# Kernel tuning notes

Hardware: AMD Instinct MI355X
Metric: run time of the kernel (lower is better)

## Reference

```python
import jax, jax.numpy as jnp
import numpy as np

NUM_HEADS, NUM_KEYS, NUM_VALUES, NUM_OUTPUTS = 8, 64, 64, 512
B, H, W, C = 16, 64, 64, 512


def setup_inputs() -> dict:
    key = jax.random.key(0)
    ks = jax.random.split(key, 5)
    def xavier(k, shape):
        fan_in, fan_out = shape
        lim = np.sqrt(6.0 / (fan_in + fan_out))
        return jax.random.uniform(k, shape, jnp.float32, -lim, lim)
    return {
        "x": jax.random.normal(ks[0], (B, H, W, C), jnp.float32),
        "Wq": xavier(ks[1], (C, NUM_HEADS * NUM_KEYS)),
        "bq": jnp.zeros((NUM_HEADS * NUM_KEYS,), jnp.float32),
        "Wk": xavier(ks[2], (C, NUM_HEADS * NUM_KEYS)),
        "bk": jnp.zeros((NUM_HEADS * NUM_KEYS,), jnp.float32),
        "Wv": xavier(ks[3], (C, NUM_HEADS * NUM_VALUES)),
        "bv": jnp.zeros((NUM_HEADS * NUM_VALUES,), jnp.float32),
        "Wo": xavier(ks[4], (NUM_VALUES, NUM_OUTPUTS)),
        "bo": jnp.zeros((NUM_OUTPUTS,), jnp.float32),
    }


def reference(x, Wq, bq, Wk, bk, Wv, bv, Wo, bo):
    b, h, w, c = x.shape
    n, dk, dv = NUM_HEADS, NUM_KEYS, NUM_VALUES
    # single pooled query per image
    q = (jnp.mean(x, axis=(1, 2)) @ Wq + bq).reshape(b, n, dk)      # [B,N,dk]
    K = (x @ Wk + bk).reshape(b, h, w, n, dk)                        # [B,H,W,N,dk]
    V = (x @ Wv + bv).reshape(b, h, w, n, dv)                        # [B,H,W,N,dv]
    scale = 1.0 / jnp.sqrt(jnp.float32(dk))
    # scores of the single query against every pixel
    s = jnp.einsum('bnk,bhwnk->bnhw', q, K) * scale                  # [B,N,H,W]
    attn_h = jax.nn.softmax(s, axis=-1)   # per row, softmax over width
    attn_v = jax.nn.softmax(s, axis=-2)   # per column, softmax over height
    A_h = jnp.einsum('bnhw,bhwnv->bnhv', attn_h, V)                  # [B,N,H,dv]
    A_v = jnp.einsum('bnhw,bhwnv->bnwv', attn_v, V)                  # [B,N,W,dv]
    # outer-product combine over spatial dims, summed over heads
    A = jnp.einsum('bnhv,bnwv->bhwv', A_h, A_v)                      # [B,H,W,dv]
    return A @ Wo + bo                                               # [B,H,W,num_outputs]
```

## Files before the change

kernel.cpp:

```cpp
#include <hip/hip_runtime.h>
#include <hip/hip_bf16.h>

#define NHEADS 8
#define DK 64
#define DV 64
#define CIN 512
#define PIX_PER_IMG 4096
#define NPIX 65536

typedef short bf16x8 __attribute__((ext_vector_type(8)));
typedef float f32x4 __attribute__((ext_vector_type(4)));

__device__ __forceinline__ float b2f(unsigned int u) {
  union { unsigned int i; float f; } v; v.i = u << 16; return v.f;
}
__device__ __forceinline__ unsigned short f2b(float f) {
  union { float f; unsigned int i; } v; v.f = f;
  unsigned int x = v.i;
  return (unsigned short)((x + 0x7fffu + ((x >> 16) & 1u)) >> 16);
}
__device__ __forceinline__ void gload_lds16(const void* g, void* l) {
  __builtin_amdgcn_global_load_lds(
      (const __attribute__((address_space(1))) void*)g,
      (__attribute__((address_space(3))) void*)l, 16, 0, 0);
}

__global__ void k_pool_convert(const float* __restrict__ x,
                               unsigned short* __restrict__ xb,
                               float* __restrict__ partial) {
  int blk = blockIdx.x;
  int b = blk >> 6, chunk = blk & 63;
  int t = threadIdx.x;
  int c4 = t & 127;
  int half = t >> 7;
  size_t rowbase = (size_t)b * PIX_PER_IMG + chunk * 64;
  const float4* x4 = (const float4*)x;
  float4 acc = make_float4(0.f, 0.f, 0.f, 0.f);
#pragma unroll 4
  for (int i = 0; i < 32; ++i) {
    int p = 2 * i + half;
    float4 v = x4[(rowbase + p) * 128 + c4];
    acc.x += v.x; acc.y += v.y; acc.z += v.z; acc.w += v.w;
    uint2 o;
    o.x = (unsigned)f2b(v.x) | ((unsigned)f2b(v.y) << 16);
    o.y = (unsigned)f2b(v.z) | ((unsigned)f2b(v.w) << 16);
    *(uint2*)(xb + (rowbase + p) * CIN + c4 * 4) = o;
  }
  *(float4*)(partial + ((size_t)(blk * 2 + half)) * CIN + c4 * 4) = acc;
}

__global__ void k_qp2(const float* __restrict__ partial,
                      const float* __restrict__ Wq, const float* __restrict__ bq,
                      const float* __restrict__ Wk, const float* __restrict__ bk,
                      float* __restrict__ P, float* __restrict__ s0) {
  __shared__ float xs[CIN];
  __shared__ float red[256];
  __shared__ float qsh[64];
  int b = blockIdx.x, n = blockIdx.y, t = threadIdx.x;
  for (int c = t; c < CIN; c += 256) {
    float s = 0.f;
    for (int ch = 0; ch < 128; ++ch) s += partial[((size_t)(b * 128 + ch)) * CIN + c];
    xs[c] = s * (1.0f / 4096.0f);
  }
  __syncthreads();
  int jj = t & 63, part = t >> 6;
  {
    float acc = 0.f;
    const float* wp = Wq + (size_t)(part * 128) * CIN + n * 64 + jj;
    for (int ci = 0; ci < 128; ++ci)
      acc += xs[part * 128 + ci] * wp[(size_t)ci * CIN];
    red[t] = acc;
  }
  __syncthreads();
  if (t < 64)
    qsh[t] = red[t] + red[t + 64] + red[t + 128] + red[t + 192] + bq[n * 64 + t];
  __syncthreads();
  if (t == 0) {
    float s = 0.f;
    for (int k = 0; k < 64; ++k) s += qsh[k] * bk[n * 64 + k];
    s0[b * NHEADS + n] = s;
  }
  for (int c = t; c < CIN; c += 256) {
    float acc = 0.f;
    const float* wr = Wk + (size_t)c * CIN + n * 64;
    for (int k = 0; k < 64; ++k) acc += qsh[k] * wr[k];
    P[((size_t)(b * NHEADS + n)) * CIN + c] = acc;
  }
}

__global__ void k_prep_w(const float* __restrict__ Wv, const float* __restrict__ Wo,
                         unsigned short* __restrict__ WvT, unsigned short* __restrict__ WoT) {
  int idx = blockIdx.x * 256 + threadIdx.x;
  if (idx < 262144) {
    int n = idx >> 9, c = idx & 511;
    WvT[idx] = f2b(Wv[(size_t)c * 512 + n]);
  } else {
    int j = idx - 262144;
    int o = j >> 6, kk = j & 63;
    WoT[j] = f2b(Wo[(size_t)kk * 512 + o]);
  }
}

__global__ void k_scores(const unsigned short* __restrict__ xb,
                         const float* __restrict__ P, const float* __restrict__ s0,
                         float* __restrict__ s) {
  __shared__ float Pl[NHEADS * 516];
  __shared__ float s0l[NHEADS];
  int blk = blockIdx.x;
  int b = blk >> 7, tile = blk & 127;
  int t = threadIdx.x;
  for (int idx = t; idx < NHEADS * CIN; idx += 256) {
    int n = idx >> 9, c = idx & 511;
    Pl[n * 516 + c] = P[((size_t)(b * NHEADS + n)) * CIN + c];
  }
  if (t < NHEADS) s0l[t] = s0[b * NHEADS + t];
  __syncthreads();
  int pl = t >> 3, n = t & 7;
  int pix = tile * 32 + pl;
  const uint4* xr = (const uint4*)(xb + ((size_t)b * PIX_PER_IMG + pix) * CIN);
  const float* Pr = Pl + n * 516;
  float acc = s0l[n];
  for (int cc = 0; cc < 64; ++cc) {
    uint4 u = xr[cc];
    int c = cc * 8;
    acc += b2f(u.x & 0xffff) * Pr[c + 0];
    acc += b2f(u.x >> 16) * Pr[c + 1];
    acc += b2f(u.y & 0xffff) * Pr[c + 2];
    acc += b2f(u.y >> 16) * Pr[c + 3];
    acc += b2f(u.z & 0xffff) * Pr[c + 4];
    acc += b2f(u.z >> 16) * Pr[c + 5];
    acc += b2f(u.w & 0xffff) * Pr[c + 6];
    acc += b2f(u.w >> 16) * Pr[c + 7];
  }
  s[((size_t)(b * NHEADS + n)) * PIX_PER_IMG + pix] = acc * 0.125f;
}

__global__ void k_softmax(const float* __restrict__ s,
                          float* __restrict__ ah, float* __restrict__ avT) {
  __shared__ float st[4096];
  int bn = blockIdx.x, t = threadIdx.x;
  const float* sp = s + (size_t)bn * 4096;
  for (int i = t; i < 4096; i += 256) st[i] = sp[i];
  __syncthreads();
  if (t < 64) {
    int h = t;
    float m = -1e30f;
    for (int w = 0; w < 64; ++w) m = fmaxf(m, st[h * 64 + w]);
    float sum = 0.f;
    for (int w = 0; w < 64; ++w) sum += __expf(st[h * 64 + w] - m);
    float inv = 1.f / sum;
    for (int w = 0; w < 64; ++w)
      ah[(size_t)bn * 4096 + h * 64 + w] = __expf(st[h * 64 + w] - m) * inv;
  } else if (t < 128) {
    int w = t - 64;
    float m = -1e30f;
    for (int h = 0; h < 64; ++h) m = fmaxf(m, st[h * 64 + w]);
    float sum = 0.f;
    for (int h = 0; h < 64; ++h) sum += __expf(st[h * 64 + w] - m);
    float inv = 1.f / sum;
    for (int h = 0; h < 64; ++h)
      avT[(size_t)bn * 4096 + w * 64 + h] = __expf(st[h * 64 + w] - m) * inv;
  }
}

__global__ void k_xh(const unsigned short* __restrict__ xb,
                     const float* __restrict__ ahg,
                     unsigned short* __restrict__ XHV) {
  __shared__ unsigned short xs[64 * 256];
  __shared__ float ahl[NHEADS * 64];
  int bh = blockIdx.x, ch = blockIdx.y, t = threadIdx.x;
  int b = bh >> 6, h = bh & 63;
  const unsigned short* src = xb + ((size_t)(b * PIX_PER_IMG + h * 64)) * CIN + ch * 256;
#pragma unroll
  for (int i = 0; i < 8; ++i) {
    int idx = i * 256 + t;
    int w = idx >> 5, off = idx & 31;
    ((uint4*)xs)[idx] = ((const uint4*)(src + (size_t)w * CIN))[off];
  }
#pragma unroll
  for (int i = 0; i < 2; ++i) {
    int idx = i * 256 + t;
    ahl[idx] = ahg[((size_t)(b * NHEADS + (idx >> 6))) * PIX_PER_IMG + h * 64 + (idx & 63)];
  }
  __syncthreads();
  int n = t >> 5, oct = t & 31;
  float acc[8] = {0.f, 0.f, 0.f, 0.f, 0.f, 0.f, 0.f, 0.f};
  const float* ar = ahl + n * 64;
  for (int w = 0; w < 64; ++w) {
    float aw = ar[w];
    uint4 u = *(const uint4*)(xs + (size_t)w * 256 + oct * 8);
    acc[0] += aw * b2f(u.x & 0xffff);
    acc[1] += aw * b2f(u.x >> 16);
    acc[2] += aw * b2f(u.y & 0xffff);
    acc[3] += aw * b2f(u.y >> 16);
    acc[4] += aw * b2f(u.z & 0xffff);
    acc[5] += aw * b2f(u.z >> 16);
    acc[6] += aw * b2f(u.w & 0xffff);
    acc[7] += aw * b2f(u.w >> 16);
  }
  uint4 o;
  o.x = (unsigned)f2b(acc[0]) | ((unsigned)f2b(acc[1]) << 16);
  o.y = (unsigned)f2b(acc[2]) | ((unsigned)f2b(acc[3]) << 16);
  o.z = (unsigned)f2b(acc[4]) | ((unsigned)f2b(acc[5]) << 16);
  o.w = (unsigned)f2b(acc[6]) | ((unsigned)f2b(acc[7]) << 16);
  size_t dst = ((size_t)(n * 2048 + b * 64 + h)) * CIN + ch * 256 + oct * 8;
  *(uint4*)(XHV + dst) = o;
}

__global__ void k_xv(const unsigned short* __restrict__ xb,
                     const float* __restrict__ avTg,
                     unsigned short* __restrict__ XHV) {
  __shared__ unsigned short xs[64 * 256];
  __shared__ float avl[NHEADS * 64];
  int bw = blockIdx.x, ch = blockIdx.y, t = threadIdx.x;
  int b = bw >> 6, w = bw & 63;
#pragma unroll
  for (int i = 0; i < 8; ++i) {
    int idx = i * 256 + t;
    int h = idx >> 5, off = idx & 31;
    ((uint4*)xs)[idx] =
        ((const uint4*)(xb + ((size_t)(b * PIX_PER_IMG + h * 64 + w)) * CIN + ch * 256))[off];
  }
#pragma unroll
  for (int i = 0; i < 2; ++i) {
    int idx = i * 256 + t;
    avl[idx] = avTg[((size_t)(b * NHEADS + (idx >> 6))) * PIX_PER_IMG + w * 64 + (idx & 63)];
  }
  __syncthreads();
  int n = t >> 5, oct = t & 31;
  float acc[8] = {0.f, 0.f, 0.f, 0.f, 0.f, 0.f, 0.f, 0.f};
  const float* ar = avl + n * 64;
  for (int h = 0; h < 64; ++h) {
    float aw = ar[h];
    uint4 u = *(const uint4*)(xs + (size_t)h * 256 + oct * 8);
    acc[0] += aw * b2f(u.x & 0xffff);
    acc[1] += aw * b2f(u.x >> 16);
    acc[2] += aw * b2f(u.y & 0xffff);
    acc[3] += aw * b2f(u.y >> 16);
    acc[4] += aw * b2f(u.z & 0xffff);
    acc[5] += aw * b2f(u.z >> 16);
    acc[6] += aw * b2f(u.w & 0xffff);
    acc[7] += aw * b2f(u.w >> 16);
  }
  uint4 o;
  o.x = (unsigned)f2b(acc[0]) | ((unsigned)f2b(acc[1]) << 16);
  o.y = (unsigned)f2b(acc[2]) | ((unsigned)f2b(acc[3]) << 16);
  o.z = (unsigned)f2b(acc[4]) | ((unsigned)f2b(acc[5]) << 16);
  o.w = (unsigned)f2b(acc[6]) | ((unsigned)f2b(acc[7]) << 16);
  size_t dst = ((size_t)(n * 2048 + 1024 + b * 64 + w)) * CIN + ch * 256 + oct * 8;
  *(uint4*)(XHV + dst) = o;
}

__global__ void k_gemm2(const unsigned short* __restrict__ XHV,
                        const unsigned short* __restrict__ WvT,
                        const float* __restrict__ bv,
                        float* __restrict__ Ah, float* __restrict__ Av) {
  __shared__ __align__(16) unsigned short As[128 * 64];
  __shared__ __align__(16) unsigned short Bs[64 * 64];
  const int t = threadIdx.x;
  const int wave = t >> 6, lane = t & 63;
  const int mtile = blockIdx.x, head = blockIdx.y;
  const int m0 = mtile * 128;
  const unsigned short* A = XHV + (size_t)head * 2048 * CIN;
  const unsigned short* BT = WvT + (size_t)head * 64 * CIN;

  f32x4 acc[2][4];
  for (int i = 0; i < 2; ++i)
    for (int j = 0; j < 4; ++j) acc[i][j] = (f32x4){0.f, 0.f, 0.f, 0.f};

  const int lrow = wave * 8 + (lane >> 3);
  const int lcolb = (lane & 7) * 16;

  for (int kt = 0; kt < 8; ++kt) {
    __syncthreads();
#pragma unroll
    for (int j = 0; j < 4; ++j) {
      gload_lds16((const char*)A + ((size_t)(m0 + j * 32 + lrow) * CIN + kt * 64) * 2 + lcolb,
                  (char*)As + (j * 32 + wave * 8) * 128);
    }
#pragma unroll
    for (int j = 0; j < 2; ++j) {
      gload_lds16((const char*)BT + ((size_t)(j * 32 + lrow) * CIN + kt * 64) * 2 + lcolb,
                  (char*)Bs + (j * 32 + wave * 8) * 128);
    }
    __syncthreads();
#pragma unroll
    for (int s = 0; s < 2; ++s) {
      bf16x8 af[2], bg[4];
#pragma unroll
      for (int i = 0; i < 2; ++i) {
        int mrow = wave * 32 + i * 16 + (lane & 15);
        af[i] = *(const bf16x8*)((const char*)As + mrow * 128 + s * 64 + ((lane >> 4) * 16));
      }
#pragma unroll
      for (int j = 0; j < 4; ++j) {
        int nrow = j * 16 + (lane & 15);
        bg[j] = *(const bf16x8*)((const char*)Bs + nrow * 128 + s * 64 + ((lane >> 4) * 16));
      }
#pragma unroll
      for (int i = 0; i < 2; ++i)
#pragma unroll
        for (int j = 0; j < 4; ++j)
          acc[i][j] = __builtin_amdgcn_mfma_f32_16x16x32_bf16(af[i], bg[j], acc[i][j], 0, 0, 0);
    }
  }
#pragma unroll
  for (int i = 0; i < 2; ++i)
#pragma unroll
    for (int j = 0; j < 4; ++j) {
      int v = j * 16 + (lane & 15);
      float bb = bv[head * 64 + v];
#pragma unroll
      for (int r = 0; r < 4; ++r) {
        int m = m0 + wave * 32 + i * 16 + ((lane >> 4) * 4) + r;
        float val = acc[i][j][r] + bb;
        if (m < 1024) {
          int b = m >> 6, h = m & 63;
          Ah[((size_t)(b * NHEADS + head)) * 4096 + h * 64 + v] = val;
        } else {
          int m2 = m - 1024;
          int b = m2 >> 6, w = m2 & 63;
          Av[((size_t)(b * NHEADS + head)) * 4096 + w * 64 + v] = val;
        }
      }
    }
}

__global__ void k_outgemm(const float* __restrict__ Ah, const float* __restrict__ Av,
                          const unsigned short* __restrict__ WoT,
                          const float* __restrict__ bo, float* __restrict__ out) {
  __shared__ __align__(16) unsigned short As[128 * 64];
  __shared__ __align__(16) unsigned short Bs[128 * 64];
  const int t = threadIdx.x;
  const int wave = t >> 6, lane = t & 63;
  const int wr = wave >> 1, wc = wave & 1;
  const int m0 = blockIdx.y * 128, n0 = blockIdx.x * 128;
  const int b = m0 >> 12, h0 = (m0 >> 6) & 63;

  const int srow = wave * 32 + (lane >> 3), scolb = (lane & 7) * 16;
#pragma unroll
  for (int j = 0; j < 4; ++j)
    gload_lds16((const char*)WoT + ((size_t)(n0 + srow + j * 8) * 64) * 2 + scolb,
                (char*)Bs + wave * 4096 + j * 1024);

  {
    const int v = t & 63, rg = t >> 6;
    float ahv0[8], ahv1[8];
#pragma unroll
    for (int n = 0; n < 8; ++n) {
      ahv0[n] = Ah[((size_t)((b * 8 + n) * 64 + h0)) * 64 + v];
      ahv1[n] = Ah[((size_t)((b * 8 + n) * 64 + h0 + 1)) * 64 + v];
    }
#pragma unroll 2
    for (int i = 0; i < 16; ++i) {
      int w = rg * 16 + i;
      float a0 = 0.f, a1 = 0.f;
#pragma unroll
      for (int n = 0; n < 8; ++n) {
        float av = Av[((size_t)((b * 8 + n) * 64 + w)) * 64 + v];
        a0 += ahv0[n] * av;
        a1 += ahv1[n] * av;
      }
      As[w * 64 + v] = f2b(a0);
      As[(64 + w) * 64 + v] = f2b(a1);
    }
  }
  __syncthreads();

  f32x4 acc[4][4];
  for (int i = 0; i < 4; ++i)
    for (int j = 0; j < 4; ++j) acc[i][j] = (f32x4){0.f, 0.f, 0.f, 0.f};
#pragma unroll
  for (int s = 0; s < 2; ++s) {
    bf16x8 af[4], bg[4];
#pragma unroll
    for (int i = 0; i < 4; ++i) {
      int mrow = wr * 64 + i * 16 + (lane & 15);
      af[i] = *(const bf16x8*)((const char*)As + mrow * 128 + s * 64 + ((lane >> 4) * 16));
    }
#pragma unroll
    for (int j = 0; j < 4; ++j) {
      int nrow = wc * 64 + j * 16 + (lane & 15);
      bg[j] = *(const bf16x8*)((const char*)Bs + nrow * 128 + s * 64 + ((lane >> 4) * 16));
    }
#pragma unroll
    for (int i = 0; i < 4; ++i)
#pragma unroll
      for (int j = 0; j < 4; ++j)
        acc[i][j] = __builtin_amdgcn_mfma_f32_16x16x32_bf16(af[i], bg[j], acc[i][j], 0, 0, 0);
  }
#pragma unroll
  for (int i = 0; i < 4; ++i)
#pragma unroll
    for (int j = 0; j < 4; ++j) {
      int mbase = m0 + wr * 64 + i * 16 + ((lane >> 4) * 4);
      int n = n0 + wc * 64 + j * 16 + (lane & 15);
      float bb = bo[n];
#pragma unroll
      for (int r = 0; r < 4; ++r)
        out[(size_t)(mbase + r) * 512 + n] = acc[i][j][r] + bb;
    }
}

extern "C" void kernel_launch(void* const* d_in, const int* in_sizes, int n_in,
                              void* d_out, int out_size, void* d_ws, size_t ws_size,
                              hipStream_t stream) {
  (void)in_sizes; (void)n_in; (void)out_size; (void)ws_size;
  const float* x = (const float*)d_in[0];
  const float* Wq = (const float*)d_in[1];
  const float* bq = (const float*)d_in[2];
  const float* Wk = (const float*)d_in[3];
  const float* bk = (const float*)d_in[4];
  const float* Wv = (const float*)d_in[5];
  const float* bv = (const float*)d_in[6];
  const float* Wo = (const float*)d_in[7];
  const float* bo = (const float*)d_in[8];
  float* out = (float*)d_out;

  char* ws = (char*)d_ws;
  unsigned short* xb = (unsigned short*)(ws + 0);
  float* s = (float*)(ws + 67108864);
  float* partial = (float*)(ws + 69206016);
  float* P = (float*)(ws + 73400320);
  float* s0 = (float*)(ws + 73662464);
  float* attn_h = (float*)(ws + 73662976);
  float* avT = (float*)(ws + 75760128);
  unsigned short* XHV = (unsigned short*)(ws + 77857280);
  float* Ah = (float*)(ws + 94634496);
  float* Av = (float*)(ws + 96731648);
  unsigned short* WvT = (unsigned short*)(ws + 98828800);
  unsigned short* WoT = (unsigned short*)(ws + 99353088);

  k_pool_convert<<<1024, 256, 0, stream>>>(x, xb, partial);
  k_qp2<<<dim3(16, 8), 256, 0, stream>>>(partial, Wq, bq, Wk, bk, P, s0);
  k_prep_w<<<1152, 256, 0, stream>>>(Wv, Wo, WvT, WoT);
  k_scores<<<2048, 256, 0, stream>>>(xb, P, s0, s);
  k_softmax<<<128, 256, 0, stream>>>(s, attn_h, avT);
  k_xh<<<dim3(1024, 2), 256, 0, stream>>>(xb, attn_h, XHV);
  k_xv<<<dim3(1024, 2), 256, 0, stream>>>(xb, avT, XHV);
  k_gemm2<<<dim3(16, 8), 256, 0, stream>>>(XHV, WvT, bv, Ah, Av);
  k_outgemm<<<dim3(4, 512), 256, 0, stream>>>(Ah, Av, WoT, bo, out);
}
```

Measured before the change: 370.9 us.

## Use MFMA split-bf16 for scores, merge launches, parallelize softmax

Computes attention scores with bf16 MFMA using a hi/lo split of the projected query to keep precision, replacing the scalar dot-product loop. It merges weight prep into the pooling kernel and the row and column weighted-sum kernels into one launch, which cuts launch count. Softmax now uses 256 threads with register buffers and shuffle reductions instead of 128 serial threads. The bk-dependent constant is dropped because softmax is invariant to a per-row shift. The hi/lo split doubles MFMA work, and the scores still read x only in bf16.

```diff
diff --git a/kernel.cpp b/kernel.cpp
--- a/kernel.cpp
+++ b/kernel.cpp
@@ -25,19 +25,33 @@
       (__attribute__((address_space(3))) void*)l, 16, 0, 0);
 }
 
-__global__ void k_pool_convert(const float* __restrict__ x,
-                               unsigned short* __restrict__ xb,
-                               float* __restrict__ partial) {
+__global__ __launch_bounds__(256) void k_pool_prep(
+    const float* __restrict__ x, unsigned short* __restrict__ xb,
+    float* __restrict__ partial,
+    const float* __restrict__ Wv, const float* __restrict__ Wo,
+    unsigned short* __restrict__ WvT, unsigned short* __restrict__ WoT) {
   int blk = blockIdx.x;
-  int b = blk >> 6, chunk = blk & 63;
   int t = threadIdx.x;
+  if (blk >= 2048) {
+    int idx = (blk - 2048) * 256 + t;
+    if (idx < 262144) {
+      int n = idx >> 9, c = idx & 511;
+      WvT[idx] = f2b(Wv[(size_t)c * 512 + n]);
+    } else {
+      int j = idx - 262144;
+      int o = j >> 6, kk = j & 63;
+      WoT[j] = f2b(Wo[(size_t)kk * 512 + o]);
+    }
+    return;
+  }
+  int b = blk >> 7, chunk = blk & 127;
   int c4 = t & 127;
   int half = t >> 7;
-  size_t rowbase = (size_t)b * PIX_PER_IMG + chunk * 64;
+  size_t rowbase = (size_t)b * PIX_PER_IMG + chunk * 32;
   const float4* x4 = (const float4*)x;
   float4 acc = make_float4(0.f, 0.f, 0.f, 0.f);
-#pragma unroll 4
-  for (int i = 0; i < 32; ++i) {
+#pragma unroll
+  for (int i = 0; i < 16; ++i) {
     int p = 2 * i + half;
     float4 v = x4[(rowbase + p) * 128 + c4];
     acc.x += v.x; acc.y += v.y; acc.z += v.z; acc.w += v.w;
@@ -49,17 +63,17 @@
   *(float4*)(partial + ((size_t)(blk * 2 + half)) * CIN + c4 * 4) = acc;
 }
 
-__global__ void k_qp2(const float* __restrict__ partial,
-                      const float* __restrict__ Wq, const float* __restrict__ bq,
-                      const float* __restrict__ Wk, const float* __restrict__ bk,
-                      float* __restrict__ P, float* __restrict__ s0) {
+__global__ __launch_bounds__(256) void k_qp2(
+    const float* __restrict__ partial,
+    const float* __restrict__ Wq, const float* __restrict__ bq,
+    const float* __restrict__ Wk, float* __restrict__ P) {
   __shared__ float xs[CIN];
   __shared__ float red[256];
   __shared__ float qsh[64];
   int b = blockIdx.x, n = blockIdx.y, t = threadIdx.x;
   for (int c = t; c < CIN; c += 256) {
     float s = 0.f;
-    for (int ch = 0; ch < 128; ++ch) s += partial[((size_t)(b * 128 + ch)) * CIN + c];
+    for (int ch = 0; ch < 256; ++ch) s += partial[((size_t)(b * 256 + ch)) * CIN + c];
     xs[c] = s * (1.0f / 4096.0f);
   }
   __syncthreads();
@@ -75,11 +89,6 @@
   if (t < 64)
     qsh[t] = red[t] + red[t + 64] + red[t + 128] + red[t + 192] + bq[n * 64 + t];
   __syncthreads();
-  if (t == 0) {
-    float s = 0.f;
-    for (int k = 0; k < 64; ++k) s += qsh[k] * bk[n * 64 + k];
-    s0[b * NHEADS + n] = s;
-  }
   for (int c = t; c < CIN; c += 256) {
     float acc = 0.f;
     const float* wr = Wk + (size_t)c * CIN + n * 64;
@@ -88,107 +97,113 @@
   }
 }
 
-__global__ void k_prep_w(const float* __restrict__ Wv, const float* __restrict__ Wo,
-                         unsigned short* __restrict__ WvT, unsigned short* __restrict__ WoT) {
-  int idx = blockIdx.x * 256 + threadIdx.x;
-  if (idx < 262144) {
-    int n = idx >> 9, c = idx & 511;
-    WvT[idx] = f2b(Wv[(size_t)c * 512 + n]);
-  } else {
-    int j = idx - 262144;
-    int o = j >> 6, kk = j & 63;
-    WoT[j] = f2b(Wo[(size_t)kk * 512 + o]);
-  }
-}
-
-__global__ void k_scores(const unsigned short* __restrict__ xb,
-                         const float* __restrict__ P, const float* __restrict__ s0,
-                         float* __restrict__ s) {
-  __shared__ float Pl[NHEADS * 516];
-  __shared__ float s0l[NHEADS];
+__global__ __launch_bounds__(256) void k_scores(
+    const unsigned short* __restrict__ xb, const float* __restrict__ P,
+    float* __restrict__ s) {
+  __shared__ __align__(16) unsigned short Pl[24 * 520];
   int blk = blockIdx.x;
-  int b = blk >> 7, tile = blk & 127;
+  int b = blk >> 6, tile = blk & 63;
   int t = threadIdx.x;
-  for (int idx = t; idx < NHEADS * CIN; idx += 256) {
-    int n = idx >> 9, c = idx & 511;
-    Pl[n * 516 + c] = P[((size_t)(b * NHEADS + n)) * CIN + c];
-  }
-  if (t < NHEADS) s0l[t] = s0[b * NHEADS + t];
-  __syncthreads();
-  int pl = t >> 3, n = t & 7;
-  int pix = tile * 32 + pl;
-  const uint4* xr = (const uint4*)(xb + ((size_t)b * PIX_PER_IMG + pix) * CIN);
-  const float* Pr = Pl + n * 516;
-  float acc = s0l[n];
-  for (int cc = 0; cc < 64; ++cc) {
-    uint4 u = xr[cc];
-    int c = cc * 8;
-    acc += b2f(u.x & 0xffff) * Pr[c + 0];
-    acc += b2f(u.x >> 16) * Pr[c + 1];
-    acc += b2f(u.y & 0xffff) * Pr[c + 2];
-    acc += b2f(u.y >> 16) * Pr[c + 3];
-    acc += b2f(u.z & 0xffff) * Pr[c + 4];
-    acc += b2f(u.z >> 16) * Pr[c + 5];
-    acc += b2f(u.w & 0xffff) * Pr[c + 6];
-    acc += b2f(u.w >> 16) * Pr[c + 7];
-  }
-  s[((size_t)(b * NHEADS + n)) * PIX_PER_IMG + pix] = acc * 0.125f;
-}
-
-__global__ void k_softmax(const float* __restrict__ s,
-                          float* __restrict__ ah, float* __restrict__ avT) {
+  for (int i = t; i < 4096; i += 256) {
+    int n = i >> 9, c = i & 511;
+    float pv = P[((size_t)(b * NHEADS + n)) * CIN + c];
+    unsigned short h = f2b(pv);
+    Pl[n * 520 + c] = h;
+    Pl[(n + 8) * 520 + c] = f2b(pv - b2f(h));
+  }
+  __syncthreads();
+  int wave = t >> 6, lane = t & 63;
+  int prow = lane & 15, kgrp = lane >> 4;
+  const unsigned short* arow =
+      xb + ((size_t)b * PIX_PER_IMG + tile * 64 + wave * 16 + prow) * CIN + kgrp * 8;
+  const unsigned short* bhi = Pl + prow * 520 + kgrp * 8;
+  const unsigned short* blo = Pl + (prow + 8) * 520 + kgrp * 8;
+  f32x4 acc = (f32x4){0.f, 0.f, 0.f, 0.f};
+#pragma unroll
+  for (int kb = 0; kb < 16; ++kb) {
+    bf16x8 af = *(const bf16x8*)(arow + kb * 32);
+    bf16x8 bh = *(const bf16x8*)(bhi + kb * 32);
+    bf16x8 bl = *(const bf16x8*)(blo + kb * 32);
+    acc = __builtin_amdgcn_mfma_f32_16x16x32_bf16(af, bh, acc, 0, 0, 0);
+    acc = __builtin_amdgcn_mfma_f32_16x16x32_bf16(af, bl, acc, 0, 0, 0);
+  }
+  int n = prow;
+  if (n < 8) {
+    float* sp = s + ((size_t)(b * NHEADS + n)) * PIX_PER_IMG + tile * 64 + wave * 16 + kgrp * 4;
+#pragma unroll
+    for (int r = 0; r < 4; ++r) sp[r] = acc[r] * 0.125f;
+  }
+}
+
+__global__ __launch_bounds__(256) void k_softmax(
+    const float* __restrict__ s, float* __restrict__ ah, float* __restrict__ avT) {
   __shared__ float st[4096];
   int bn = blockIdx.x, t = threadIdx.x;
   const float* sp = s + (size_t)bn * 4096;
   for (int i = t; i < 4096; i += 256) st[i] = sp[i];
   __syncthreads();
-  if (t < 64) {
-    int h = t;
-    float m = -1e30f;
-    for (int w = 0; w < 64; ++w) m = fmaxf(m, st[h * 64 + w]);
-    float sum = 0.f;
-    for (int w = 0; w < 64; ++w) sum += __expf(st[h * 64 + w] - m);
-    float inv = 1.f / sum;
-    for (int w = 0; w < 64; ++w)
-      ah[(size_t)bn * 4096 + h * 64 + w] = __expf(st[h * 64 + w] - m) * inv;
-  } else if (t < 128) {
-    int w = t - 64;
-    float m = -1e30f;
-    for (int h = 0; h < 64; ++h) m = fmaxf(m, st[h * 64 + w]);
-    float sum = 0.f;
-    for (int h = 0; h < 64; ++h) sum += __expf(st[h * 64 + w] - m);
-    float inv = 1.f / sum;
-    for (int h = 0; h < 64; ++h)
-      avT[(size_t)bn * 4096 + w * 64 + h] = __expf(st[h * 64 + w] - m) * inv;
-  }
-}
-
-__global__ void k_xh(const unsigned short* __restrict__ xb,
-                     const float* __restrict__ ahg,
-                     unsigned short* __restrict__ XHV) {
+  int task = t >> 1, half = t & 1;
+  int id = task & 63;
+  bool isRow = task < 64;
+  float v[32];
+#pragma unroll
+  for (int i = 0; i < 32; ++i) {
+    int e = half * 32 + i;
+    v[i] = isRow ? st[id * 64 + e] : st[e * 64 + id];
+  }
+  float m = -1e30f;
+#pragma unroll
+  for (int i = 0; i < 32; ++i) m = fmaxf(m, v[i]);
+  m = fmaxf(m, __shfl_xor(m, 1));
+  float sum = 0.f;
+#pragma unroll
+  for (int i = 0; i < 32; ++i) { v[i] = __expf(v[i] - m); sum += v[i]; }
+  sum += __shfl_xor(sum, 1);
+  float inv = 1.f / sum;
+  float* dst = (isRow ? ah : avT) + (size_t)bn * 4096 + id * 64 + half * 32;
+#pragma unroll
+  for (int i = 0; i < 32; ++i) dst[i] = v[i] * inv;
+}
+
+__global__ __launch_bounds__(256) void k_xhv(
+    const unsigned short* __restrict__ xb, const float* __restrict__ ahg,
+    const float* __restrict__ avTg, unsigned short* __restrict__ XHV) {
   __shared__ unsigned short xs[64 * 256];
-  __shared__ float ahl[NHEADS * 64];
-  int bh = blockIdx.x, ch = blockIdx.y, t = threadIdx.x;
-  int b = bh >> 6, h = bh & 63;
-  const unsigned short* src = xb + ((size_t)(b * PIX_PER_IMG + h * 64)) * CIN + ch * 256;
-#pragma unroll
-  for (int i = 0; i < 8; ++i) {
-    int idx = i * 256 + t;
-    int w = idx >> 5, off = idx & 31;
-    ((uint4*)xs)[idx] = ((const uint4*)(src + (size_t)w * CIN))[off];
-  }
+  __shared__ float al[NHEADS * 64];
+  int bx = blockIdx.x, ch = blockIdx.y, t = threadIdx.x;
+  bool isV = bx >= 1024;
+  int bi = isV ? bx - 1024 : bx;
+  int b = bi >> 6, rc = bi & 63;
+  if (!isV) {
+    const unsigned short* src = xb + ((size_t)(b * PIX_PER_IMG + rc * 64)) * CIN + ch * 256;
+#pragma unroll
+    for (int i = 0; i < 8; ++i) {
+      int idx = i * 256 + t;
+      int w = idx >> 5, off = idx & 31;
+      ((uint4*)xs)[idx] = ((const uint4*)(src + (size_t)w * CIN))[off];
+    }
+  } else {
+#pragma unroll
+    for (int i = 0; i < 8; ++i) {
+      int idx = i * 256 + t;
+      int h = idx >> 5, off = idx & 31;
+      ((uint4*)xs)[idx] =
+          ((const uint4*)(xb + ((size_t)(b * PIX_PER_IMG + h * 64 + rc)) * CIN + ch * 256))[off];
+    }
+  }
+  const float* ag = isV ? avTg : ahg;
 #pragma unroll
   for (int i = 0; i < 2; ++i) {
     int idx = i * 256 + t;
-    ahl[idx] = ahg[((size_t)(b * NHEADS + (idx >> 6))) * PIX_PER_IMG + h * 64 + (idx & 63)];
+    al[idx] = ag[((size_t)(b * NHEADS + (idx >> 6))) * PIX_PER_IMG + rc * 64 + (idx & 63)];
   }
   __syncthreads();
   int n = t >> 5, oct = t & 31;
   float acc[8] = {0.f, 0.f, 0.f, 0.f, 0.f, 0.f, 0.f, 0.f};
-  const float* ar = ahl + n * 64;
-  for (int w = 0; w < 64; ++w) {
-    float aw = ar[w];
-    uint4 u = *(const uint4*)(xs + (size_t)w * 256 + oct * 8);
+  const float* ar = al + n * 64;
+  for (int p = 0; p < 64; ++p) {
+    float aw = ar[p];
+    uint4 u = *(const uint4*)(xs + (size_t)p * 256 + oct * 8);
     acc[0] += aw * b2f(u.x & 0xffff);
     acc[1] += aw * b2f(u.x >> 16);
     acc[2] += aw * b2f(u.y & 0xffff);
@@ -203,58 +218,13 @@
   o.y = (unsigned)f2b(acc[2]) | ((unsigned)f2b(acc[3]) << 16);
   o.z = (unsigned)f2b(acc[4]) | ((unsigned)f2b(acc[5]) << 16);
   o.w = (unsigned)f2b(acc[6]) | ((unsigned)f2b(acc[7]) << 16);
-  size_t dst = ((size_t)(n * 2048 + b * 64 + h)) * CIN + ch * 256 + oct * 8;
+  size_t dst = ((size_t)(n * 2048 + (isV ? 1024 : 0) + b * 64 + rc)) * CIN + ch * 256 + oct * 8;
   *(uint4*)(XHV + dst) = o;
 }
 
-__global__ void k_xv(const unsigned short* __restrict__ xb,
-                     const float* __restrict__ avTg,
-                     unsigned short* __restrict__ XHV) {
-  __shared__ unsigned short xs[64 * 256];
-  __shared__ float avl[NHEADS * 64];
-  int bw = blockIdx.x, ch = blockIdx.y, t = threadIdx.x;
-  int b = bw >> 6, w = bw & 63;
-#pragma unroll
-  for (int i = 0; i < 8; ++i) {
-    int idx = i * 256 + t;
-    int h = idx >> 5, off = idx & 31;
-    ((uint4*)xs)[idx] =
-        ((const uint4*)(xb + ((size_t)(b * PIX_PER_IMG + h * 64 + w)) * CIN + ch * 256))[off];
-  }
-#pragma unroll
-  for (int i = 0; i < 2; ++i) {
-    int idx = i * 256 + t;
-    avl[idx] = avTg[((size_t)(b * NHEADS + (idx >> 6))) * PIX_PER_IMG + w * 64 + (idx & 63)];
-  }
-  __syncthreads();
-  int n = t >> 5, oct = t & 31;
-  float acc[8] = {0.f, 0.f, 0.f, 0.f, 0.f, 0.f, 0.f, 0.f};
-  const float* ar = avl + n * 64;
-  for (int h = 0; h < 64; ++h) {
-    float aw = ar[h];
-    uint4 u = *(const uint4*)(xs + (size_t)h * 256 + oct * 8);
-    acc[0] += aw * b2f(u.x & 0xffff);
-    acc[1] += aw * b2f(u.x >> 16);
-    acc[2] += aw * b2f(u.y & 0xffff);
-    acc[3] += aw * b2f(u.y >> 16);
-    acc[4] += aw * b2f(u.z & 0xffff);
-    acc[5] += aw * b2f(u.z >> 16);
-    acc[6] += aw * b2f(u.w & 0xffff);
-    acc[7] += aw * b2f(u.w >> 16);
-  }
-  uint4 o;
-  o.x = (unsigned)f2b(acc[0]) | ((unsigned)f2b(acc[1]) << 16);
-  o.y = (unsigned)f2b(acc[2]) | ((unsigned)f2b(acc[3]) << 16);
-  o.z = (unsigned)f2b(acc[4]) | ((unsigned)f2b(acc[5]) << 16);
-  o.w = (unsigned)f2b(acc[6]) | ((unsigned)f2b(acc[7]) << 16);
-  size_t dst = ((size_t)(n * 2048 + 1024 + b * 64 + w)) * CIN + ch * 256 + oct * 8;
-  *(uint4*)(XHV + dst) = o;
-}
-
-__global__ void k_gemm2(const unsigned short* __restrict__ XHV,
-                        const unsigned short* __restrict__ WvT,
-                        const float* __restrict__ bv,
-                        float* __restrict__ Ah, float* __restrict__ Av) {
+__global__ __launch_bounds__(256) void k_gemm2(
+    const unsigned short* __restrict__ XHV, const unsigned short* __restrict__ WvT,
+    const float* __restrict__ bv, float* __restrict__ Ah, float* __restrict__ Av) {
   __shared__ __align__(16) unsigned short As[128 * 64];
   __shared__ __align__(16) unsigned short Bs[64 * 64];
   const int t = threadIdx.x;
@@ -326,9 +296,10 @@
     }
 }
 
-__global__ void k_outgemm(const float* __restrict__ Ah, const float* __restrict__ Av,
-                          const unsigned short* __restrict__ WoT,
-                          const float* __restrict__ bo, float* __restrict__ out) {
+__global__ __launch_bounds__(256) void k_outgemm(
+    const float* __restrict__ Ah, const float* __restrict__ Av,
+    const unsigned short* __restrict__ WoT,
+    const float* __restrict__ bo, float* __restrict__ out) {
   __shared__ __align__(16) unsigned short As[128 * 64];
   __shared__ __align__(16) unsigned short Bs[128 * 64];
   const int t = threadIdx.x;
@@ -410,7 +381,6 @@
   const float* Wq = (const float*)d_in[1];
   const float* bq = (const float*)d_in[2];
   const float* Wk = (const float*)d_in[3];
-  const float* bk = (const float*)d_in[4];
   const float* Wv = (const float*)d_in[5];
   const float* bv = (const float*)d_in[6];
   const float* Wo = (const float*)d_in[7];
@@ -419,25 +389,22 @@
 
   char* ws = (char*)d_ws;
   unsigned short* xb = (unsigned short*)(ws + 0);
-  float* s = (float*)(ws + 67108864);
-  float* partial = (float*)(ws + 69206016);
-  float* P = (float*)(ws + 73400320);
-  float* s0 = (float*)(ws + 73662464);
-  float* attn_h = (float*)(ws + 73662976);
-  float* avT = (float*)(ws + 75760128);
-  unsigned short* XHV = (unsigned short*)(ws + 77857280);
-  float* Ah = (float*)(ws + 94634496);
-  float* Av = (float*)(ws + 96731648);
-  unsigned short* WvT = (unsigned short*)(ws + 98828800);
-  unsigned short* WoT = (unsigned short*)(ws + 99353088);
-
-  k_pool_convert<<<1024, 256, 0, stream>>>(x, xb, partial);
-  k_qp2<<<dim3(16, 8), 256, 0, stream>>>(partial, Wq, bq, Wk, bk, P, s0);
-  k_prep_w<<<1152, 256, 0, stream>>>(Wv, Wo, WvT, WoT);
-  k_scores<<<2048, 256, 0, stream>>>(xb, P, s0, s);
+  float* partial = (float*)(ws + 67108864);
+  float* s = (float*)(ws + 75497472);
+  float* P = (float*)(ws + 77594624);
+  float* attn_h = (float*)(ws + 77856768);
+  float* avT = (float*)(ws + 79953920);
+  unsigned short* XHV = (unsigned short*)(ws + 82051072);
+  float* Ah = (float*)(ws + 98828288);
+  float* Av = (float*)(ws + 100925440);
+  unsigned short* WvT = (unsigned short*)(ws + 103022592);
+  unsigned short* WoT = (unsigned short*)(ws + 103546880);
+
+  k_pool_prep<<<3200, 256, 0, stream>>>(x, xb, partial, Wv, Wo, WvT, WoT);
+  k_qp2<<<dim3(16, 8), 256, 0, stream>>>(partial, Wq, bq, Wk, P);
+  k_scores<<<1024, 256, 0, stream>>>(xb, P, s);
   k_softmax<<<128, 256, 0, stream>>>(s, attn_h, avT);
-  k_xh<<<dim3(1024, 2), 256, 0, stream>>>(xb, attn_h, XHV);
-  k_xv<<<dim3(1024, 2), 256, 0, stream>>>(xb, avT, XHV);
+  k_xhv<<<dim3(2048, 2), 256, 0, stream>>>(xb, attn_h, avT, XHV);
   k_gemm2<<<dim3(16, 8), 256, 0, stream>>>(XHV, WvT, bv, Ah, Av);
   k_outgemm<<<dim3(4, 512), 256, 0, stream>>>(Ah, Av, WoT, bo, out);
 }
```

Result: no change. 369.7 us (-0.3%).
